# Performance work log

Hardware: AMD Instinct MI355X
Metric: run time of the kernel (lower is better)

## Reference

```python
import jax, jax.numpy as jnp
import numpy as np


def apply_rope(x):
    # x: [b, h, n, d], d even
    b, h, n, d = x.shape
    half = d // 2
    freqs = jnp.arange(0, half, dtype=x.dtype) / half
    theta = 1.0 / 10000 ** freqs                       # [half]
    positions = jnp.arange(n, dtype=x.dtype)
    angles = positions[:, None] * theta[None, :]       # [n, half]
    cos = jnp.cos(angles)[None, None, :, :]
    sin = jnp.sin(angles)[None, None, :, :]
    x1 = x[..., ::2]
    x2 = x[..., 1::2]
    r1 = x1 * cos - x2 * sin
    r2 = x1 * sin + x2 * cos
    # interleave r1, r2 back into even/odd lanes
    return jnp.stack([r1, r2], axis=-1).reshape(b, h, n, d)


def setup_inputs() -> dict:
    key = jax.random.key(0)
    ks = jax.random.split(key, 4)
    B, N, D = 2, 2048, 1024
    x = jax.random.normal(ks[0], (B, N, D), dtype=jnp.float32)
    w_qkv = jax.random.normal(ks[1], (D, 3 * D), dtype=jnp.float32) * (1.0 / np.sqrt(D))
    b_qkv = jnp.zeros((3 * D,), dtype=jnp.float32)
    w_out = jax.random.normal(ks[2], (D, D), dtype=jnp.float32) * (1.0 / np.sqrt(D))
    b_out = jnp.zeros((D,), dtype=jnp.float32)
    return {"x": x, "w_qkv": w_qkv, "b_qkv": b_qkv, "w_out": w_out, "b_out": b_out}


def reference(x, w_qkv, b_qkv, w_out, b_out):
    B, N, D = x.shape
    H = 16
    hd = D // H
    qkv = x @ w_qkv + b_qkv                            # [B, N, 3D]
    q, k, v = jnp.split(qkv, 3, axis=-1)
    # [B, N, D] -> [B, H, N, hd]
    to_heads = lambda t: t.reshape(B, N, H, hd).transpose(0, 2, 1, 3)
    q, k, v = to_heads(q), to_heads(k), to_heads(v)
    # ELU+1 feature map (applied BEFORE RoPE, as in source)
    q = jax.nn.elu(q) + 1
    k = jax.nn.elu(k) + 1
    rot_q = apply_rope(q)
    rot_k = apply_rope(k)
    attn_num = jnp.einsum('bhid,bhjd->bhij', rot_q, rot_k)   # [B,H,N,N]
    attn_denom = jnp.einsum('bhid,bhjd->bhij', q, k)         # [B,H,N,N]
    attn_weights = attn_num / attn_denom
    # dropout deterministic (train=False)
    out = jnp.einsum('bhij,bhjd->bhid', attn_weights, v)     # [B,H,N,hd]
    out = out.transpose(0, 2, 1, 3).reshape(B, N, D)
    return out @ w_out + b_out
```

## Files before the change

### kernel.cpp

```cpp
#include <hip/hip_runtime.h>
#include <hip/hip_bf16.h>

#define B_   2
#define N_   2048
#define D_   1024
#define H_   16
#define HD   64
#define HALF 32
#define M_   (B_*N_)
#define DQKV (3*D_)

typedef __bf16 bf16x8 __attribute__((ext_vector_type(8)));
typedef float  f32x4  __attribute__((ext_vector_type(4)));
typedef float  f32x16 __attribute__((ext_vector_type(16)));

__device__ __forceinline__ bf16x8 ldfrag(const char* tile, int row, int ch) {
    return *(const bf16x8*)(tile + row * 128 + (((ch) ^ (row & 7)) << 4));
}
__device__ __forceinline__ void stfrag16(char* tile, int row, int ch, uint4 v) {
    *(uint4*)(tile + row * 128 + (((ch) ^ (row & 7)) << 4)) = v;
}

__device__ __forceinline__ void gld16(const void* g, void* l) {
    __builtin_amdgcn_global_load_lds(
        (const __attribute__((address_space(1))) unsigned int*)g,
        (__attribute__((address_space(3))) unsigned int*)l, 16, 0, 0);
}

__device__ __forceinline__ unsigned pack2(float a, float b) {
    union { __hip_bfloat16 h; unsigned short s; } x, y;
    x.h = __float2bfloat16(a); y.h = __float2bfloat16(b);
    return (unsigned)x.s | ((unsigned)y.s << 16);
}

__global__ __launch_bounds__(256) void k_tables(float* __restrict__ cos_t,
                                                float* __restrict__ sin_t) {
    int i = blockIdx.x * 256 + threadIdx.x;
    if (i >= N_ * HALF) return;
    int n = i / HALF, j = i % HALF;
    float theta = powf(10000.f, -(float)j / (float)HALF);
    float ang = (float)n * theta;
    cos_t[i] = cosf(ang);
    sin_t[i] = sinf(ang);
}

__global__ __launch_bounds__(256) void k_cvt_x(const float* __restrict__ x,
                                               __hip_bfloat16* __restrict__ xb) {
    int i = blockIdx.x * 256 + threadIdx.x;
    float4 v = ((const float4*)x)[i];
    union { ushort4 u; __hip_bfloat16 h[4]; } o;
    o.h[0] = __float2bfloat16(v.x); o.h[1] = __float2bfloat16(v.y);
    o.h[2] = __float2bfloat16(v.z); o.h[3] = __float2bfloat16(v.w);
    ((ushort4*)xb)[i] = o.u;
}

__global__ __launch_bounds__(256) void k_cvt_t(const float* __restrict__ w,
                                               __hip_bfloat16* __restrict__ wt, int ncols) {
    __shared__ float tile[32][33];
    int n0 = blockIdx.x * 32, k0 = blockIdx.y * 32;
    int tx = threadIdx.x & 31, ty = threadIdx.x >> 5;
#pragma unroll
    for (int i = 0; i < 32; i += 8)
        tile[ty + i][tx] = w[(size_t)(k0 + ty + i) * ncols + n0 + tx];
    __syncthreads();
#pragma unroll
    for (int i = 0; i < 32; i += 8)
        wt[(size_t)(n0 + ty + i) * 1024 + k0 + tx] = __float2bfloat16(tile[tx][ty + i]);
}

__global__ __launch_bounds__(256) void k_qkv(
        const __hip_bfloat16* __restrict__ xb, const __hip_bfloat16* __restrict__ wqT,
        const float* __restrict__ bias,
        const float* __restrict__ cos_t, const float* __restrict__ sin_t,
        __hip_bfloat16* __restrict__ qf, __hip_bfloat16* __restrict__ kf,
        __hip_bfloat16* __restrict__ rq, __hip_bfloat16* __restrict__ rk,
        __hip_bfloat16* __restrict__ vt) {
    __shared__ __align__(16) char sA[128 * 128];
    __shared__ __align__(16) char sB[128 * 128];

    const int t    = threadIdx.x;
    const int m0   = blockIdx.y * 128;
    const int n0w  = blockIdx.x * 128;
    const int lane = t & 63;
    const int lrow = lane & 15;
    const int lgrp = lane >> 4;
    const int wid  = t >> 6;
    const int wr   = wid >> 1;
    const int wc   = wid & 1;
    const int lr8  = lane >> 3;
    const int cg   = (lane & 7) ^ lr8;

    f32x4 acc[4][4] = {};

    for (int kt = 0; kt < D_ / 64; ++kt) {
        const int k0 = kt * 64;
        __syncthreads();
#pragma unroll
        for (int it = 0; it < 4; ++it) {
            int sb  = (wid * 4 + it) * 64;
            int row = (sb >> 3) + lr8;
            gld16(xb  + (size_t)(m0  + row) * D_ + k0 + cg * 8, sA + sb * 16);
            gld16(wqT + (size_t)(n0w + row) * D_ + k0 + cg * 8, sB + sb * 16);
        }
        __syncthreads();

        bf16x8 bfr[4][2];
#pragma unroll
        for (int fn = 0; fn < 4; ++fn) {
            bfr[fn][0] = ldfrag(sB, wc * 64 + fn * 16 + lrow, lgrp);
            bfr[fn][1] = ldfrag(sB, wc * 64 + fn * 16 + lrow, 4 + lgrp);
        }
#pragma unroll
        for (int fm = 0; fm < 4; ++fm) {
            bf16x8 a0 = ldfrag(sA, wr * 64 + fm * 16 + lrow, lgrp);
            bf16x8 a1 = ldfrag(sA, wr * 64 + fm * 16 + lrow, 4 + lgrp);
#pragma unroll
            for (int fn = 0; fn < 4; ++fn) {
                acc[fm][fn] = __builtin_amdgcn_mfma_f32_16x16x32_bf16(a0, bfr[fn][0], acc[fm][fn], 0, 0, 0);
                acc[fm][fn] = __builtin_amdgcn_mfma_f32_16x16x32_bf16(a1, bfr[fn][1], acc[fm][fn], 0, 0, 0);
            }
        }
    }

#pragma unroll
    for (int fn = 0; fn < 4; ++fn) {
        int c   = n0w + wc * 64 + fn * 16 + lrow;
        int sec = c >> 10;
        int cc  = c & 1023;
        int h   = cc >> 6, dd = cc & 63;
        float bia = bias[c];
#pragma unroll
        for (int fm = 0; fm < 4; ++fm) {
            int mb = m0 + wr * 64 + fm * 16 + lgrp * 4;
            int b  = mb >> 11;
            int n  = mb & (N_ - 1);
            if (sec == 2) {
                union { ushort4 u; __hip_bfloat16 hh[4]; } pk;
#pragma unroll
                for (int r = 0; r < 4; ++r)
                    pk.hh[r] = __float2bfloat16(acc[fm][fn][r] + bia);
                *(ushort4*)(vt + ((size_t)(b * H_ + h) * HD + dd) * N_ + n) = pk.u;
            } else {
#pragma unroll
                for (int r = 0; r < 4; ++r) {
                    float val = acc[fm][fn][r] + bia;
                    float e  = val > 0.f ? val + 1.f : __expf(val);
                    float ep = __shfl_xor(e, 1);
                    int pj = dd >> 1;
                    float cs = cos_t[(n + r) * HALF + pj];
                    float sn = sin_t[(n + r) * HALF + pj];
                    float rv = (dd & 1) ? (ep * sn + e * cs) : (e * cs - ep * sn);
                    size_t o = ((size_t)(b * H_ + h) * N_ + n + r) * HD + dd;
                    if (sec == 0) { qf[o] = __float2bfloat16(e); rq[o] = __float2bfloat16(rv); }
                    else          { kf[o] = __float2bfloat16(e); rk[o] = __float2bfloat16(rv); }
                }
            }
        }
    }
}

__global__ __launch_bounds__(512, 2) void k_attn(
        const __hip_bfloat16* __restrict__ qf, const __hip_bfloat16* __restrict__ kf,
        const __hip_bfloat16* __restrict__ rq, const __hip_bfloat16* __restrict__ rk,
        const __hip_bfloat16* __restrict__ vt, __hip_bfloat16* __restrict__ ctxb) {
    __shared__ __align__(16) char sbuf[2][2][3 * 8192];

    const int t    = threadIdx.x;
    const int lane = t & 63;
    const int l31  = lane & 31;
    const int h    = lane >> 5;
    const int wid  = t >> 6;
    const int qw   = wid & 3;
    const int ks   = wid >> 2;
    const int tl   = t & 255;

    const int bid = blockIdx.x;
    const int swz = (bid & 7) * 32 + (bid >> 3);
    const int bh  = swz >> 3;
    const int q0  = (swz & 7) * 256;
    const size_t base = (size_t)bh * (N_ * HD);
    const int q0w = q0 + qw * 64;

    bf16x8 bq[2][4], bqe[2][4];
#pragma unroll
    for (int qb = 0; qb < 2; ++qb)
#pragma unroll
        for (int kc = 0; kc < 4; ++kc) {
            int row = q0w + qb * 32 + l31;
            int col = kc * 16 + h * 8;
            bq [qb][kc] = *(const bf16x8*)(rq + base + (size_t)row * HD + col);
            bqe[qb][kc] = *(const bf16x8*)(qf + base + (size_t)row * HD + col);
        }

    uint4 st[6];
    auto stage_load = [&](int k0) {
#pragma unroll
        for (int j = 0; j < 6; ++j) {
            int slot = j * 256 + tl;
            int ci = slot & 511, tile = slot >> 9;
            int row = ci >> 3, cs = ci & 7;
            int cg = cs ^ (row & 7);
            const char* g;
            if (tile == 0)      g = (const char*)(rk + base + (size_t)(k0 + row) * HD) + cg * 16;
            else if (tile == 1) g = (const char*)(kf + base + (size_t)(k0 + row) * HD) + cg * 16;
            else                g = (const char*)(vt + base + (size_t)row * N_ + k0) + cg * 16;
            st[j] = *(const uint4*)g;
        }
    };
    auto stage_write = [&](int buf) {
#pragma unroll
        for (int j = 0; j < 6; ++j) {
            int slot = j * 256 + tl;
            *(uint4*)(sbuf[ks][buf] + slot * 16) = st[j];
        }
    };

    stage_load(ks * 64);
    stage_write(0);
    __syncthreads();

    f32x16 o[2][2] = {};

    for (int r = 0; r < 16; ++r) {
        const int cur = r & 1;
        const char* Rk = sbuf[ks][cur];
        const char* Ke = Rk + 8192;
        const char* Vt = Rk + 16384;

        if (r + 1 < 16) stage_load((2 * (r + 1) + ks) * 64);

        bf16x8 wa[2][4];
#pragma unroll
        for (int kb = 0; kb < 2; ++kb) {
            bf16x8 ark[4], ake[4];
#pragma unroll
            for (int kc = 0; kc < 4; ++kc) {
                ark[kc] = ldfrag(Rk, kb * 32 + l31, kc * 2 + h);
                ake[kc] = ldfrag(Ke, kb * 32 + l31, kc * 2 + h);
            }
#pragma unroll
            for (int qb = 0; qb < 2; ++qb) {
                f32x16 num = {}, den = {};
#pragma unroll
                for (int kc = 0; kc < 4; ++kc)
                    num = __builtin_amdgcn_mfma_f32_32x32x16_bf16(ark[kc], bq[qb][kc], num, 0, 0, 0);
#pragma unroll
                for (int kc = 0; kc < 4; ++kc)
                    den = __builtin_amdgcn_mfma_f32_32x32x16_bf16(ake[kc], bqe[qb][kc], den, 0, 0, 0);
                unsigned u0 = pack2(num[0]  * __builtin_amdgcn_rcpf(den[0]),
                                    num[1]  * __builtin_amdgcn_rcpf(den[1]));
                unsigned u1 = pack2(num[2]  * __builtin_amdgcn_rcpf(den[2]),
                                    num[3]  * __builtin_amdgcn_rcpf(den[3]));
                unsigned u2 = pack2(num[4]  * __builtin_amdgcn_rcpf(den[4]),
                                    num[5]  * __builtin_amdgcn_rcpf(den[5]));
                unsigned u3 = pack2(num[6]  * __builtin_amdgcn_rcpf(den[6]),
                                    num[7]  * __builtin_amdgcn_rcpf(den[7]));
                unsigned u4 = pack2(num[8]  * __builtin_amdgcn_rcpf(den[8]),
                                    num[9]  * __builtin_amdgcn_rcpf(den[9]));
                unsigned u5 = pack2(num[10] * __builtin_amdgcn_rcpf(den[10]),
                                    num[11] * __builtin_amdgcn_rcpf(den[11]));
                unsigned u6 = pack2(num[12] * __builtin_amdgcn_rcpf(den[12]),
                                    num[13] * __builtin_amdgcn_rcpf(den[13]));
                unsigned u7 = pack2(num[14] * __builtin_amdgcn_rcpf(den[14]),
                                    num[15] * __builtin_amdgcn_rcpf(den[15]));
                asm volatile("v_permlane32_swap_b32 %0, %1" : "+v"(u0), "+v"(u2));
                asm volatile("v_permlane32_swap_b32 %0, %1" : "+v"(u1), "+v"(u3));
                asm volatile("v_permlane32_swap_b32 %0, %1" : "+v"(u4), "+v"(u6));
                asm volatile("v_permlane32_swap_b32 %0, %1" : "+v"(u5), "+v"(u7));
                union { unsigned uu[4]; bf16x8 v; } f0, f1;
                f0.uu[0] = u0; f0.uu[1] = u1; f0.uu[2] = u2; f0.uu[3] = u3;
                f1.uu[0] = u4; f1.uu[1] = u5; f1.uu[2] = u6; f1.uu[3] = u7;
                wa[qb][kb * 2 + 0] = f0.v;
                wa[qb][kb * 2 + 1] = f1.v;
            }
        }

#pragma unroll
        for (int db = 0; db < 2; ++db) {
            bf16x8 bv[4];
#pragma unroll
            for (int kc = 0; kc < 4; ++kc)
                bv[kc] = ldfrag(Vt, db * 32 + l31, kc * 2 + h);
#pragma unroll
            for (int qb = 0; qb < 2; ++qb)
#pragma unroll
                for (int kc = 0; kc < 4; ++kc)
                    o[qb][db] = __builtin_amdgcn_mfma_f32_32x32x16_bf16(wa[qb][kc], bv[kc], o[qb][db], 0, 0, 0);
        }

        if (r + 1 < 16) stage_write(cur ^ 1);
        __syncthreads();
    }

    float* sred = (float*)sbuf;
    if (ks == 1) {
#pragma unroll
        for (int qb = 0; qb < 2; ++qb)
#pragma unroll
            for (int db = 0; db < 2; ++db)
#pragma unroll
                for (int i = 0; i < 16; ++i)
                    sred[(((qw * 2 + qb) * 2 + db) << 10) + i * 64 + lane] = o[qb][db][i];
    }
    __syncthreads();
    if (ks == 0) {
#pragma unroll
        for (int qb = 0; qb < 2; ++qb)
#pragma unroll
            for (int db = 0; db < 2; ++db)
#pragma unroll
                for (int i = 0; i < 16; ++i) {
                    float v = o[qb][db][i] + sred[(((qw * 2 + qb) * 2 + db) << 10) + i * 64 + lane];
                    int qq = q0w + qb * 32 + (i & 3) + 8 * (i >> 2) + 4 * h;
                    ctxb[base + (size_t)qq * HD + db * 32 + l31] = __float2bfloat16(v);
                }
    }
}

__global__ __launch_bounds__(256) void k_proj(
        const __hip_bfloat16* __restrict__ ctxb, const __hip_bfloat16* __restrict__ woT,
        const float* __restrict__ bias, float* __restrict__ out) {
    __shared__ __align__(16) char sA[128 * 128];
    __shared__ __align__(16) char sB[128 * 128];

    const int t    = threadIdx.x;
    const int m0   = blockIdx.y * 128;
    const int n0w  = blockIdx.x * 128;
    const int lane = t & 63;
    const int lrow = lane & 15;
    const int lgrp = lane >> 4;
    const int wid  = t >> 6;
    const int wr   = wid >> 1;
    const int wc   = wid & 1;
    const int lr8  = lane >> 3;
    const int cg   = (lane & 7) ^ lr8;

    f32x4 acc[4][4] = {};

    for (int kt = 0; kt < D_ / 64; ++kt) {
        const int k0 = kt * 64;
        const int hh = k0 >> 6;
        __syncthreads();
#pragma unroll
        for (int it = 0; it < 4; ++it) {
            int sb  = (wid * 4 + it) * 64;
            int row = (sb >> 3) + lr8;
            int m = m0 + row;
            int b = m >> 11, n = m & (N_ - 1);
            gld16(ctxb + ((size_t)(b * H_ + hh) * N_ + n) * HD + cg * 8, sA + sb * 16);
            gld16(woT + (size_t)(n0w + row) * D_ + k0 + cg * 8, sB + sb * 16);
        }
        __syncthreads();

        bf16x8 bfr[4][2];
#pragma unroll
        for (int fn = 0; fn < 4; ++fn) {
            bfr[fn][0] = ldfrag(sB, wc * 64 + fn * 16 + lrow, lgrp);
            bfr[fn][1] = ldfrag(sB, wc * 64 + fn * 16 + lrow, 4 + lgrp);
        }
#pragma unroll
        for (int fm = 0; fm < 4; ++fm) {
            bf16x8 a0 = ldfrag(sA, wr * 64 + fm * 16 + lrow, lgrp);
            bf16x8 a1 = ldfrag(sA, wr * 64 + fm * 16 + lrow, 4 + lgrp);
#pragma unroll
            for (int fn = 0; fn < 4; ++fn) {
                acc[fm][fn] = __builtin_amdgcn_mfma_f32_16x16x32_bf16(a0, bfr[fn][0], acc[fm][fn], 0, 0, 0);
                acc[fm][fn] = __builtin_amdgcn_mfma_f32_16x16x32_bf16(a1, bfr[fn][1], acc[fm][fn], 0, 0, 0);
            }
        }
    }

#pragma unroll
    for (int fn = 0; fn < 4; ++fn) {
        int c = n0w + wc * 64 + fn * 16 + lrow;
        float bia = bias[c];
#pragma unroll
        for (int fm = 0; fm < 4; ++fm) {
            int m = m0 + wr * 64 + fm * 16 + lgrp * 4;
#pragma unroll
            for (int r = 0; r < 4; ++r)
                out[(size_t)(m + r) * D_ + c] = acc[fm][fn][r] + bia;
        }
    }
}

extern "C" void kernel_launch(void* const* d_in, const int* in_sizes, int n_in,
                              void* d_out, int out_size, void* d_ws, size_t ws_size,
                              hipStream_t stream) {
    const float* x     = (const float*)d_in[0];
    const float* w_qkv = (const float*)d_in[1];
    const float* b_qkv = (const float*)d_in[2];
    const float* w_out = (const float*)d_in[3];
    const float* b_out = (const float*)d_in[4];
    float* out = (float*)d_out;

    char* ws = (char*)d_ws;
    const size_t TAB  = (size_t)N_ * HALF * sizeof(float);
    const size_t HARR = (size_t)B_ * H_ * N_ * HD * 2;
    float* cos_t = (float*)ws;
    float* sin_t = (float*)(ws + TAB);
    char* p = ws + 2 * TAB;
    __hip_bfloat16* qf  = (__hip_bfloat16*)(p);            p += HARR;
    __hip_bfloat16* kf  = (__hip_bfloat16*)(p);            p += HARR;
    __hip_bfloat16* rq  = (__hip_bfloat16*)(p);            p += HARR;
    __hip_bfloat16* rk  = (__hip_bfloat16*)(p);            p += HARR;
    __hip_bfloat16* vt  = (__hip_bfloat16*)(p);            p += HARR;
    __hip_bfloat16* xb  = (__hip_bfloat16*)(p);            p += HARR;
    __hip_bfloat16* ctxb = xb;
    __hip_bfloat16* wqT = (__hip_bfloat16*)(p);            p += (size_t)DQKV * D_ * 2;
    __hip_bfloat16* woT = (__hip_bfloat16*)(p);            p += (size_t)D_ * D_ * 2;

    hipLaunchKernelGGL(k_tables, dim3((N_ * HALF + 255) / 256), dim3(256), 0, stream,
                       cos_t, sin_t);
    hipLaunchKernelGGL(k_cvt_x, dim3(M_ * D_ / 4 / 256), dim3(256), 0, stream, x, xb);
    hipLaunchKernelGGL(k_cvt_t, dim3(DQKV / 32, D_ / 32), dim3(256), 0, stream,
                       w_qkv, wqT, DQKV);
    hipLaunchKernelGGL(k_cvt_t, dim3(D_ / 32, D_ / 32), dim3(256), 0, stream,
                       w_out, woT, D_);
    hipLaunchKernelGGL(k_qkv, dim3(DQKV / 128, M_ / 128), dim3(256), 0, stream,
                       xb, wqT, b_qkv, cos_t, sin_t, qf, kf, rq, rk, vt);
    hipLaunchKernelGGL(k_attn, dim3(256), dim3(512), 0, stream,
                       qf, kf, rq, rk, vt, ctxb);
    hipLaunchKernelGGL(k_proj, dim3(D_ / 128, M_ / 128), dim3(256), 0, stream,
                       ctxb, woT, b_out, out);
}
```

Before: 178.0 us.

## Store K/V in MFMA fragment order and load directly from global in attention

The QKV kernel now writes K, K-feature and V in a fragment-major layout that matches the attention kernel's MFMA operand shape. The attention kernel drops its double-buffered LDS staging and barriers and loads each fragment straight from global memory as one contiguous 16-byte read per lane. This removes LDS traffic and per-iteration synchronisation. In exchange it relies on L2/cache for reuse across the waves of a block, and the scattered 2-byte writes in the QKV epilogue may cost more.

```diff
diff --git a/kernel.cpp b/kernel.cpp
--- a/kernel.cpp
+++ b/kernel.cpp
@@ -32,6 +32,9 @@
     x.h = __float2bfloat16(a); y.h = __float2bfloat16(b);
     return (unsigned)x.s | ((unsigned)y.s << 16);
 }
+
+#define FRAG_OFF(kt, kb, c, l31, e) \
+    ((((size_t)((kt) * 2 + (kb)) * 8 + (c)) * 32 + (l31)) * 8 + (e))
 
 __global__ __launch_bounds__(256) void k_tables(float* __restrict__ cos_t,
                                                 float* __restrict__ sin_t) {
@@ -72,9 +75,9 @@
         const __hip_bfloat16* __restrict__ xb, const __hip_bfloat16* __restrict__ wqT,
         const float* __restrict__ bias,
         const float* __restrict__ cos_t, const float* __restrict__ sin_t,
-        __hip_bfloat16* __restrict__ qf, __hip_bfloat16* __restrict__ kf,
-        __hip_bfloat16* __restrict__ rq, __hip_bfloat16* __restrict__ rk,
-        __hip_bfloat16* __restrict__ vt) {
+        __hip_bfloat16* __restrict__ qf, __hip_bfloat16* __restrict__ gke,
+        __hip_bfloat16* __restrict__ rq, __hip_bfloat16* __restrict__ gk,
+        __hip_bfloat16* __restrict__ gv) {
     __shared__ __align__(16) char sA[128 * 128];
     __shared__ __align__(16) char sB[128 * 128];
 
@@ -134,12 +137,14 @@
             int mb = m0 + wr * 64 + fm * 16 + lgrp * 4;
             int b  = mb >> 11;
             int n  = mb & (N_ - 1);
+            size_t hbase = (size_t)(b * H_ + h) * (N_ * HD);
             if (sec == 2) {
                 union { ushort4 u; __hip_bfloat16 hh[4]; } pk;
 #pragma unroll
                 for (int r = 0; r < 4; ++r)
                     pk.hh[r] = __float2bfloat16(acc[fm][fn][r] + bia);
-                *(ushort4*)(vt + ((size_t)(b * H_ + h) * HD + dd) * N_ + n) = pk.u;
+                size_t fo = FRAG_OFF(n >> 6, dd >> 5, (n & 63) >> 3, dd & 31, n & 7);
+                *(ushort4*)(gv + hbase + fo) = pk.u;
             } else {
 #pragma unroll
                 for (int r = 0; r < 4; ++r) {
@@ -150,9 +155,15 @@
                     float cs = cos_t[(n + r) * HALF + pj];
                     float sn = sin_t[(n + r) * HALF + pj];
                     float rv = (dd & 1) ? (ep * sn + e * cs) : (e * cs - ep * sn);
-                    size_t o = ((size_t)(b * H_ + h) * N_ + n + r) * HD + dd;
-                    if (sec == 0) { qf[o] = __float2bfloat16(e); rq[o] = __float2bfloat16(rv); }
-                    else          { kf[o] = __float2bfloat16(e); rk[o] = __float2bfloat16(rv); }
+                    if (sec == 0) {
+                        size_t o = hbase + (size_t)(n + r) * HD + dd;
+                        qf[o] = __float2bfloat16(e); rq[o] = __float2bfloat16(rv);
+                    } else {
+                        size_t fo = FRAG_OFF(n >> 6, (n >> 5) & 1, dd >> 3,
+                                             (n & 31) + r, dd & 7);
+                        gke[hbase + fo] = __float2bfloat16(e);
+                        gk [hbase + fo] = __float2bfloat16(rv);
+                    }
                 }
             }
         }
@@ -160,10 +171,10 @@
 }
 
 __global__ __launch_bounds__(512, 2) void k_attn(
-        const __hip_bfloat16* __restrict__ qf, const __hip_bfloat16* __restrict__ kf,
-        const __hip_bfloat16* __restrict__ rq, const __hip_bfloat16* __restrict__ rk,
-        const __hip_bfloat16* __restrict__ vt, __hip_bfloat16* __restrict__ ctxb) {
-    __shared__ __align__(16) char sbuf[2][2][3 * 8192];
+        const __hip_bfloat16* __restrict__ qf, const __hip_bfloat16* __restrict__ gke,
+        const __hip_bfloat16* __restrict__ rq, const __hip_bfloat16* __restrict__ gk,
+        const __hip_bfloat16* __restrict__ gv, __hip_bfloat16* __restrict__ ctxb) {
+    __shared__ float sred[16384];
 
     const int t    = threadIdx.x;
     const int lane = t & 63;
@@ -172,7 +183,6 @@
     const int wid  = t >> 6;
     const int qw   = wid & 3;
     const int ks   = wid >> 2;
-    const int tl   = t & 255;
 
     const int bid = blockIdx.x;
     const int swz = (bid & 7) * 32 + (bid >> 3);
@@ -192,42 +202,14 @@
             bqe[qb][kc] = *(const bf16x8*)(qf + base + (size_t)row * HD + col);
         }
 
-    uint4 st[6];
-    auto stage_load = [&](int k0) {
-#pragma unroll
-        for (int j = 0; j < 6; ++j) {
-            int slot = j * 256 + tl;
-            int ci = slot & 511, tile = slot >> 9;
-            int row = ci >> 3, cs = ci & 7;
-            int cg = cs ^ (row & 7);
-            const char* g;
-            if (tile == 0)      g = (const char*)(rk + base + (size_t)(k0 + row) * HD) + cg * 16;
-            else if (tile == 1) g = (const char*)(kf + base + (size_t)(k0 + row) * HD) + cg * 16;
-            else                g = (const char*)(vt + base + (size_t)row * N_ + k0) + cg * 16;
-            st[j] = *(const uint4*)g;
-        }
-    };
-    auto stage_write = [&](int buf) {
-#pragma unroll
-        for (int j = 0; j < 6; ++j) {
-            int slot = j * 256 + tl;
-            *(uint4*)(sbuf[ks][buf] + slot * 16) = st[j];
-        }
-    };
-
-    stage_load(ks * 64);
-    stage_write(0);
-    __syncthreads();
+    const __hip_bfloat16* K  = gk  + base;
+    const __hip_bfloat16* Ke = gke + base;
+    const __hip_bfloat16* V  = gv  + base;
 
     f32x16 o[2][2] = {};
 
     for (int r = 0; r < 16; ++r) {
-        const int cur = r & 1;
-        const char* Rk = sbuf[ks][cur];
-        const char* Ke = Rk + 8192;
-        const char* Vt = Rk + 16384;
-
-        if (r + 1 < 16) stage_load((2 * (r + 1) + ks) * 64);
+        const int kt = 2 * r + ks;
 
         bf16x8 wa[2][4];
 #pragma unroll
@@ -235,8 +217,9 @@
             bf16x8 ark[4], ake[4];
 #pragma unroll
             for (int kc = 0; kc < 4; ++kc) {
-                ark[kc] = ldfrag(Rk, kb * 32 + l31, kc * 2 + h);
-                ake[kc] = ldfrag(Ke, kb * 32 + l31, kc * 2 + h);
+                size_t fo = FRAG_OFF(kt, kb, kc * 2 + h, l31, 0);
+                ark[kc] = *(const bf16x8*)(K  + fo);
+                ake[kc] = *(const bf16x8*)(Ke + fo);
             }
 #pragma unroll
             for (int qb = 0; qb < 2; ++qb) {
@@ -280,19 +263,15 @@
             bf16x8 bv[4];
 #pragma unroll
             for (int kc = 0; kc < 4; ++kc)
-                bv[kc] = ldfrag(Vt, db * 32 + l31, kc * 2 + h);
+                bv[kc] = *(const bf16x8*)(V + FRAG_OFF(kt, db, kc * 2 + h, l31, 0));
 #pragma unroll
             for (int qb = 0; qb < 2; ++qb)
 #pragma unroll
                 for (int kc = 0; kc < 4; ++kc)
                     o[qb][db] = __builtin_amdgcn_mfma_f32_32x32x16_bf16(wa[qb][kc], bv[kc], o[qb][db], 0, 0, 0);
         }
-
-        if (r + 1 < 16) stage_write(cur ^ 1);
-        __syncthreads();
-    }
-
-    float* sred = (float*)sbuf;
+    }
+
     if (ks == 1) {
 #pragma unroll
         for (int qb = 0; qb < 2; ++qb)
@@ -401,10 +380,10 @@
     float* sin_t = (float*)(ws + TAB);
     char* p = ws + 2 * TAB;
     __hip_bfloat16* qf  = (__hip_bfloat16*)(p);            p += HARR;
-    __hip_bfloat16* kf  = (__hip_bfloat16*)(p);            p += HARR;
+    __hip_bfloat16* gke = (__hip_bfloat16*)(p);            p += HARR;
     __hip_bfloat16* rq  = (__hip_bfloat16*)(p);            p += HARR;
-    __hip_bfloat16* rk  = (__hip_bfloat16*)(p);            p += HARR;
-    __hip_bfloat16* vt  = (__hip_bfloat16*)(p);            p += HARR;
+    __hip_bfloat16* gk  = (__hip_bfloat16*)(p);            p += HARR;
+    __hip_bfloat16* gv  = (__hip_bfloat16*)(p);            p += HARR;
     __hip_bfloat16* xb  = (__hip_bfloat16*)(p);            p += HARR;
     __hip_bfloat16* ctxb = xb;
     __hip_bfloat16* wqT = (__hip_bfloat16*)(p);            p += (size_t)DQKV * D_ * 2;
@@ -418,9 +397,9 @@
     hipLaunchKernelGGL(k_cvt_t, dim3(D_ / 32, D_ / 32), dim3(256), 0, stream,
                        w_out, woT, D_);
     hipLaunchKernelGGL(k_qkv, dim3(DQKV / 128, M_ / 128), dim3(256), 0, stream,
-                       xb, wqT, b_qkv, cos_t, sin_t, qf, kf, rq, rk, vt);
+                       xb, wqT, b_qkv, cos_t, sin_t, qf, gke, rq, gk, gv);
     hipLaunchKernelGGL(k_attn, dim3(256), dim3(512), 0, stream,
-                       qf, kf, rq, rk, vt, ctxb);
+                       qf, gke, rq, gk, gv, ctxb);
     hipLaunchKernelGGL(k_proj, dim3(D_ / 128, M_ / 128), dim3(256), 0, stream,
                        ctxb, woT, b_out, out);
 }
```

After: 189.9 us. 6.7% more time.
